# Optimization experiments

Measured on AMD Instinct MI355X. Metric: run time of the kernel, lower is better.

## Reference

```python
import jax, jax.numpy as jnp
import numpy as np

CL = 32      # config.cl (latent width)
NOBJ = 32    # config.num_obj
N = 1024     # batch


def _linear_params(key, fan_in, fan_out):
    w = jax.random.normal(key, (fan_in, fan_out), dtype=jnp.float32) / np.sqrt(fan_in)
    b = jnp.full((fan_out,), 0.1, dtype=jnp.float32)
    return w, b


def setup_inputs() -> dict:
    key = jax.random.key(0)
    keys = jax.random.split(key, 16)
    inp = {"s": jax.random.normal(keys[0], (N, NOBJ, CL // 2), dtype=jnp.float32)}
    specs = [
        ("state_enc", [(CL // 2, CL)]),
        ("self", [(CL, CL), (CL, CL)]),
        ("rel", [(2 * CL + 1, 2 * CL), (2 * CL, CL), (CL, CL)]),
        ("att", [(2 * CL + 1, 2 * CL), (2 * CL, CL), (CL, 1)]),
        ("aff", [(CL, CL), (CL, CL), (CL, CL)]),
        ("out", [(2 * CL, CL), (CL, CL)]),
    ]
    k = 1
    for name, shapes in specs:
        for j, (fi, fo) in enumerate(shapes):
            w, b = _linear_params(keys[k], fi, fo)
            k += 1
            if len(shapes) == 1:
                inp[name + "_w"], inp[name + "_b"] = w, b
            else:
                inp[name + "_w" + str(j)], inp[name + "_b" + str(j)] = w, b
    inp["core_idx"] = 0
    return inp


def _forward(s, state_enc_w, state_enc_b,
             self_w0, self_b0, self_w1, self_b1,
             rel_w0, rel_b0, rel_w1, rel_b1, rel_w2, rel_b2,
             att_w0, att_b0, att_w1, att_b1, att_w2, att_b2,
             aff_w0, aff_b0, aff_w1, aff_b1, aff_w2, aff_b2,
             out_w0, out_b0, out_w1, out_b1):
    # state encoding; keep raw (x, y) positions in the first 2 channels
    enc = s @ state_enc_w + state_enc_b                      # (n, o, cl)
    s2 = jnp.concatenate([s[..., :2], enc[..., 2:]], axis=-1)  # (n, o, cl)

    # self dynamics (residual MLP)
    h1 = jax.nn.relu(s2 @ self_w0 + self_b0)
    self_dyn = h1 @ self_w1 + self_b1 + h1                   # (n, o, cl)

    # pairwise squared distance over first two channels
    pos = s2[..., :2]
    diff = pos[:, :, None, :] - pos[:, None, :, :]           # (n, o, o, 2)
    dist = jnp.sum(diff * diff, axis=-1)                     # (n, o, o)

    # first layer of the edge MLPs applied to cat(obj_i, obj_j, dist) without
    # materializing the (n, o, o, 2cl+1) concat: split weight into W_i|W_j|w_d
    def pair_first(W, b):
        a = s2 @ W[:CL]                                      # (n, o, H)
        c = s2 @ W[CL:2 * CL]                                # (n, o, H)
        return a[:, :, None, :] + c[:, None, :, :] + dist[..., None] * W[2 * CL] + b

    # relation core (residual on last layer)
    rel1 = jax.nn.relu(pair_first(rel_w0, rel_b0))           # (n, o, o, 2cl)
    rel2 = jax.nn.relu(rel1 @ rel_w1 + rel_b1)               # (n, o, o, cl)
    rel_f = rel2 @ rel_w2 + rel_b2 + rel2                    # (n, o, o, cl)

    # attention net -> exp (unnormalized attention)
    att = jax.nn.relu(pair_first(att_w0, att_b0))
    att = jax.nn.relu(att @ att_w1 + att_b1)
    att = jnp.exp(att @ att_w2 + att_b2)                     # (n, o, o, 1)

    diag_mask = (1.0 - jnp.eye(NOBJ, dtype=s2.dtype))[None, :, :, None]
    rel_dyn = jnp.sum(rel_f * diag_mask * att, axis=2)       # (n, o, cl)

    dyn = self_dyn + rel_dyn

    # affector (tanh residual MLP)
    aff1 = jnp.tanh(dyn @ aff_w0 + aff_b0)
    aff2 = jnp.tanh(aff1 @ aff_w1 + aff_b1) + aff1
    aff3 = aff2 @ aff_w2 + aff_b2

    # output head
    aff_s = jnp.concatenate([aff3, s2], axis=-1)             # (n, o, 2cl)
    o1 = jnp.tanh(aff_s @ out_w0 + out_b0)
    result = o1 @ out_w1 + out_b1 + o1                       # (n, o, cl)
    return result


def reference(s, state_enc_w, state_enc_b,
              self_w0, self_b0, self_w1, self_b1,
              rel_w0, rel_b0, rel_w1, rel_b1, rel_w2, rel_b2,
              att_w0, att_b0, att_w1, att_b1, att_w2, att_b2,
              aff_w0, aff_b0, aff_w1, aff_b1, aff_w2, aff_b2,
              out_w0, out_b0, out_w1, out_b1, core_idx):
    # core_idx selects one of 3 identical cores in the original; only core 0
    # is materialized here (forward uses a single core).
    del core_idx
    return _forward(s, state_enc_w, state_enc_b,
                    self_w0, self_b0, self_w1, self_b1,
                    rel_w0, rel_b0, rel_w1, rel_b1, rel_w2, rel_b2,
                    att_w0, att_b0, att_w1, att_b1, att_w2, att_b2,
                    aff_w0, aff_b0, aff_w1, aff_b1, aff_w2, aff_b2,
                    out_w0, out_b0, out_w1, out_b1)
```

## Files before the change

### kernel.cpp

```cpp
#include <hip/hip_runtime.h>
#include <stdint.h>


enum : int {
  ENC_W  = 0,     ENC_B  = 512,
  SELF_W0 = 544,  SELF_B0 = 1568, SELF_W1 = 1600, SELF_B1 = 2624,
  REL_W0 = 2656,  REL_B0 = 6816,  REL_W1 = 6880,  REL_B1 = 8928,
  REL_W2 = 8960,  REL_B2 = 9984,
  ATT_W0 = 10016, ATT_B0 = 14176, ATT_W1 = 14240, ATT_B1 = 16288,
  ATT_W2 = 16320, ATT_B2 = 16352,
  AFF_W0 = 16356, AFF_B0 = 17380, AFF_W1 = 17412, AFF_B1 = 18436,
  AFF_W2 = 18468, AFF_B2 = 19492,
  OUT_W0 = 19524, OUT_B0 = 21572, OUT_W1 = 21604, OUT_B1 = 22628,
  W_FLAG = 22660,
  W_TOTAL = 22661
};

__device__ __forceinline__ float bf2f(uint16_t h) {
  union { uint32_t u; float f; } v; v.u = ((uint32_t)h) << 16; return v.f;
}
__device__ __forceinline__ uint16_t f2bf(float f) {
  union { float f; uint32_t u; } v; v.f = f;
  uint32_t r = (v.u + 0x7fffu + ((v.u >> 16) & 1u)) >> 16;
  return (uint16_t)r;
}

struct ConvArgs {
  const void* src[28];
  const uint32_t* probe;
  int size[28];
  int off[28];
};

__global__ void dyn_conv_kernel(ConvArgs a, float* __restrict__ W) {
  const int t = blockIdx.x;
  const bool is_fp32 = (*a.probe == 0x3DCCCCCDu);
  const int cnt = a.size[t];
  float* d = W + a.off[t];
  if (is_fp32) {
    const float* s = (const float*)a.src[t];
    for (int e = threadIdx.x; e < cnt; e += blockDim.x) d[e] = s[e];
  } else {
    const uint16_t* s = (const uint16_t*)a.src[t];
    for (int e = threadIdx.x; e < cnt; e += blockDim.x) d[e] = bf2f(s[e]);
  }
  if (t == 0 && threadIdx.x == 0) W[W_FLAG] = is_fp32 ? 1.f : 0.f;
}

struct ArenaPair {
  float pa[32][68];
  float pc[32][68];
};
struct ArenaPost {
  float rd[32][36];
  float t1[32][36];
  float t2[32][36];
};
struct ArenaEarly {
  float s[32][16];
  float h1[32][33];
};
union ArenaU {
  ArenaPair a;
  ArenaPost b;
  ArenaEarly c;
};

__global__ __launch_bounds__(256, 2) void dyn_main_kernel(
    const void* __restrict__ Sv,
    const float* __restrict__ Wf,
    void* __restrict__ OUTv)
{
  __shared__ __align__(16) ArenaU u;
  __shared__ float sh_s2[32][33];
  __shared__ float sh_dist[32][33];
  __shared__ float sh_sd[32][33];
  __shared__ float sh_wdr[64];
  __shared__ float sh_wda[64];
  __shared__ __align__(16) float shW1[2048];
  __shared__ float sh_misc[100];

  const int tid = threadIdx.x;
  const int n   = blockIdx.x;
  const int i8  = tid >> 3;
  const int l8  = tid & 7;
  const int m0  = l8 << 2;

  const bool is_fp32 = (Wf[W_FLAG] != 0.f);

  {
    const int e = tid * 2;
    if (is_fp32) {
      const float* sp = (const float*)Sv + (size_t)n * 512;
      u.c.s[e >> 4][e & 15]             = sp[e];
      u.c.s[(e + 1) >> 4][(e + 1) & 15] = sp[e + 1];
    } else {
      const uint16_t* sp = (const uint16_t*)Sv + (size_t)n * 512;
      u.c.s[e >> 4][e & 15]             = bf2f(sp[e]);
      u.c.s[(e + 1) >> 4][(e + 1) & 15] = bf2f(sp[e + 1]);
    }
  }
  __syncthreads();

  {
    float e0 = Wf[ENC_B + m0 + 0], e1 = Wf[ENC_B + m0 + 1];
    float e2 = Wf[ENC_B + m0 + 2], e3 = Wf[ENC_B + m0 + 3];
    #pragma unroll
    for (int c = 0; c < 16; ++c) {
      const float sc = u.c.s[i8][c];
      const float4 w = *(const float4*)&Wf[ENC_W + c * 32 + m0];
      e0 = fmaf(sc, w.x, e0); e1 = fmaf(sc, w.y, e1);
      e2 = fmaf(sc, w.z, e2); e3 = fmaf(sc, w.w, e3);
    }
    if (m0 == 0) { e0 = u.c.s[i8][0]; e1 = u.c.s[i8][1]; }
    sh_s2[i8][m0 + 0] = e0; sh_s2[i8][m0 + 1] = e1;
    sh_s2[i8][m0 + 2] = e2; sh_s2[i8][m0 + 3] = e3;
  }
  __syncthreads();

  {
    const float xi = sh_s2[i8][0], yi = sh_s2[i8][1];
    #pragma unroll
    for (int q = 0; q < 4; ++q) {
      const int j = m0 + q;
      const float dx = xi - sh_s2[j][0];
      const float dy = yi - sh_s2[j][1];
      sh_dist[i8][j] = dx * dx + dy * dy;
    }
  }
  {
    float a0 = Wf[SELF_B0 + m0 + 0], a1 = Wf[SELF_B0 + m0 + 1];
    float a2 = Wf[SELF_B0 + m0 + 2], a3 = Wf[SELF_B0 + m0 + 3];
    #pragma unroll
    for (int k = 0; k < 32; ++k) {
      const float x = sh_s2[i8][k];
      const float4 w = *(const float4*)&Wf[SELF_W0 + k * 32 + m0];
      a0 = fmaf(x, w.x, a0); a1 = fmaf(x, w.y, a1);
      a2 = fmaf(x, w.z, a2); a3 = fmaf(x, w.w, a3);
    }
    u.c.h1[i8][m0 + 0] = fmaxf(a0, 0.f); u.c.h1[i8][m0 + 1] = fmaxf(a1, 0.f);
    u.c.h1[i8][m0 + 2] = fmaxf(a2, 0.f); u.c.h1[i8][m0 + 3] = fmaxf(a3, 0.f);
  }
  __syncthreads();

  {
    float a0 = Wf[SELF_B1 + m0 + 0], a1 = Wf[SELF_B1 + m0 + 1];
    float a2 = Wf[SELF_B1 + m0 + 2], a3 = Wf[SELF_B1 + m0 + 3];
    #pragma unroll
    for (int k = 0; k < 32; ++k) {
      const float x = u.c.h1[i8][k];
      const float4 w = *(const float4*)&Wf[SELF_W1 + k * 32 + m0];
      a0 = fmaf(x, w.x, a0); a1 = fmaf(x, w.y, a1);
      a2 = fmaf(x, w.z, a2); a3 = fmaf(x, w.w, a3);
    }
    sh_sd[i8][m0 + 0] = a0 + u.c.h1[i8][m0 + 0];
    sh_sd[i8][m0 + 1] = a1 + u.c.h1[i8][m0 + 1];
    sh_sd[i8][m0 + 2] = a2 + u.c.h1[i8][m0 + 2];
    sh_sd[i8][m0 + 3] = a3 + u.c.h1[i8][m0 + 3];
  }
  __syncthreads();

  auto precompute_ac = [&](int W0base, int B0base) {
    const int arr = tid >> 7;
    const int row = (tid >> 2) & 31;
    const int k0  = (tid & 3) * 16;
    const float* bb = Wf + B0base + k0;
    const float bs = (arr == 0) ? 1.f : 0.f;
    float acc[16];
    #pragma unroll
    for (int kk = 0; kk < 16; ++kk) acc[kk] = bs * bb[kk];
    const float* wb = Wf + W0base + arr * 2048 + k0;
    for (int c = 0; c < 32; ++c) {
      const float sc = sh_s2[row][c];
      const float* w = wb + c * 64;
      #pragma unroll
      for (int kk = 0; kk < 16; kk += 4) {
        const float4 wv = *(const float4*)&w[kk];
        acc[kk + 0] = fmaf(sc, wv.x, acc[kk + 0]);
        acc[kk + 1] = fmaf(sc, wv.y, acc[kk + 1]);
        acc[kk + 2] = fmaf(sc, wv.z, acc[kk + 2]);
        acc[kk + 3] = fmaf(sc, wv.w, acc[kk + 3]);
      }
    }
    float* dst = (arr == 0) ? &u.a.pa[row][k0] : &u.a.pc[row][k0];
    #pragma unroll
    for (int kk = 0; kk < 16; kk += 4)
      *(float4*)&dst[kk] = make_float4(acc[kk], acc[kk+1], acc[kk+2], acc[kk+3]);
  };

  if (tid < 64)        sh_wdr[tid]      = Wf[REL_W0 + 64 * 64 + tid];
  else if (tid < 128)  sh_wda[tid - 64] = Wf[ATT_W0 + 64 * 64 + (tid - 64)];
  ((float4*)shW1)[tid]       = *(const float4*)&Wf[ATT_W1 + tid * 4];
  ((float4*)shW1)[tid + 256] = *(const float4*)&Wf[ATT_W1 + (tid + 256) * 4];
  if (tid < 97)
    sh_misc[tid] = Wf[tid < 32 ? REL_B1 + tid
                    : tid < 64 ? ATT_B1 + (tid - 32)
                    : tid < 96 ? ATT_W2 + (tid - 64) : ATT_B2];
  precompute_ac(ATT_W0, ATT_B0);
  __syncthreads();

  auto att_pair = [&](int p) -> float {
    asm volatile("" ::: "memory");
    const int j = l8 + 8 * p;
    const float d = sh_dist[i8][j];
    const float4* A = (const float4*)&u.a.pa[i8][0];
    const float4* C = (const float4*)&u.a.pc[j][0];
    const float4* D = (const float4*)&sh_wda[0];
    float v[32];
    #pragma unroll
    for (int m = 0; m < 32; ++m) v[m] = sh_misc[32 + m];
    #pragma unroll 1
    for (int kq = 0; kq < 16; ++kq) {
      const float4 av = A[kq], cv = C[kq], wv = D[kq];
      const float x0 = fmaxf(fmaf(d, wv.x, av.x + cv.x), 0.f);
      const float x1 = fmaxf(fmaf(d, wv.y, av.y + cv.y), 0.f);
      const float x2 = fmaxf(fmaf(d, wv.z, av.z + cv.z), 0.f);
      const float x3 = fmaxf(fmaf(d, wv.w, av.w + cv.w), 0.f);
      const float4* wb = (const float4*)shW1 + kq * 32;
      #pragma unroll
      for (int mq = 0; mq < 8; ++mq) {
        const float4 w0 = wb[mq], w1 = wb[8+mq], w2 = wb[16+mq], w3 = wb[24+mq];
        float t;
        t = fmaf(x0, w0.x, v[mq*4+0]); t = fmaf(x1, w1.x, t);
        t = fmaf(x2, w2.x, t);         v[mq*4+0] = fmaf(x3, w3.x, t);
        t = fmaf(x0, w0.y, v[mq*4+1]); t = fmaf(x1, w1.y, t);
        t = fmaf(x2, w2.y, t);         v[mq*4+1] = fmaf(x3, w3.y, t);
        t = fmaf(x0, w0.z, v[mq*4+2]); t = fmaf(x1, w1.z, t);
        t = fmaf(x2, w2.z, t);         v[mq*4+2] = fmaf(x3, w3.z, t);
        t = fmaf(x0, w0.w, v[mq*4+3]); t = fmaf(x1, w1.w, t);
        t = fmaf(x2, w2.w, t);         v[mq*4+3] = fmaf(x3, w3.w, t);
      }
    }
    float s0 = sh_misc[96], s1 = 0.f, s2 = 0.f, s3 = 0.f;
    #pragma unroll
    for (int k = 0; k < 32; k += 4) {
      s0 = fmaf(fmaxf(v[k + 0], 0.f), sh_misc[64 + k + 0], s0);
      s1 = fmaf(fmaxf(v[k + 1], 0.f), sh_misc[64 + k + 1], s1);
      s2 = fmaf(fmaxf(v[k + 2], 0.f), sh_misc[64 + k + 2], s2);
      s3 = fmaf(fmaxf(v[k + 3], 0.f), sh_misc[64 + k + 3], s3);
    }
    const float lg = (s0 + s1) + (s2 + s3);
    return (j == i8) ? 0.f : expf(lg);
  };
  const float e0 = att_pair(0);
  const float e1 = att_pair(1);
  const float e2 = att_pair(2);
  const float e3 = att_pair(3);
  float E = (e0 + e1) + (e2 + e3);
  __syncthreads();

  ((float4*)shW1)[tid]       = *(const float4*)&Wf[REL_W1 + tid * 4];
  ((float4*)shW1)[tid + 256] = *(const float4*)&Wf[REL_W1 + (tid + 256) * 4];
  precompute_ac(REL_W0, REL_B0);
  __syncthreads();

  float g[32];
  #pragma unroll
  for (int m = 0; m < 32; ++m) g[m] = 0.f;

  auto rel_pair = [&](int p, float e) {
    asm volatile("" ::: "memory");
    const int j = l8 + 8 * p;
    const float d = sh_dist[i8][j];
    const float4* A = (const float4*)&u.a.pa[i8][0];
    const float4* C = (const float4*)&u.a.pc[j][0];
    const float4* D = (const float4*)&sh_wdr[0];
    float v[32];
    #pragma unroll
    for (int m = 0; m < 32; ++m) v[m] = sh_misc[m];
    #pragma unroll 1
    for (int kq = 0; kq < 16; ++kq) {
      const float4 av = A[kq], cv = C[kq], wv = D[kq];
      const float x0 = fmaxf(fmaf(d, wv.x, av.x + cv.x), 0.f);
      const float x1 = fmaxf(fmaf(d, wv.y, av.y + cv.y), 0.f);
      const float x2 = fmaxf(fmaf(d, wv.z, av.z + cv.z), 0.f);
      const float x3 = fmaxf(fmaf(d, wv.w, av.w + cv.w), 0.f);
      const float4* wb = (const float4*)shW1 + kq * 32;
      #pragma unroll
      for (int mq = 0; mq < 8; ++mq) {
        const float4 w0 = wb[mq], w1 = wb[8+mq], w2 = wb[16+mq], w3 = wb[24+mq];
        float t;
        t = fmaf(x0, w0.x, v[mq*4+0]); t = fmaf(x1, w1.x, t);
        t = fmaf(x2, w2.x, t);         v[mq*4+0] = fmaf(x3, w3.x, t);
        t = fmaf(x0, w0.y, v[mq*4+1]); t = fmaf(x1, w1.y, t);
        t = fmaf(x2, w2.y, t);         v[mq*4+1] = fmaf(x3, w3.y, t);
        t = fmaf(x0, w0.z, v[mq*4+2]); t = fmaf(x1, w1.z, t);
        t = fmaf(x2, w2.z, t);         v[mq*4+2] = fmaf(x3, w3.z, t);
        t = fmaf(x0, w0.w, v[mq*4+3]); t = fmaf(x1, w1.w, t);
        t = fmaf(x2, w2.w, t);         v[mq*4+3] = fmaf(x3, w3.w, t);
      }
    }
    #pragma unroll
    for (int m = 0; m < 32; ++m)
      g[m] = fmaf(e, fmaxf(v[m], 0.f), g[m]);
  };
  rel_pair(0, e0);
  rel_pair(1, e1);
  rel_pair(2, e2);
  rel_pair(3, e3);

  #pragma unroll
  for (int m = 0; m < 32; ++m) {
    float vv = g[m];
    vv += __shfl_xor(vv, 1);
    vv += __shfl_xor(vv, 2);
    vv += __shfl_xor(vv, 4);
    g[m] = vv;
  }
  E += __shfl_xor(E, 1);
  E += __shfl_xor(E, 2);
  E += __shfl_xor(E, 4);
  __syncthreads();
  if (l8 == 0) {
    #pragma unroll
    for (int q = 0; q < 8; ++q)
      *(float4*)&u.b.t1[i8][q * 4] =
          make_float4(g[q * 4], g[q * 4 + 1], g[q * 4 + 2], g[q * 4 + 3]);
    u.b.t1[i8][32] = E;
  }
  __syncthreads();

  {
    const float Ei = u.b.t1[i8][32];
    float a0 = fmaf(Ei, Wf[REL_B2 + m0 + 0], u.b.t1[i8][m0 + 0]);
    float a1 = fmaf(Ei, Wf[REL_B2 + m0 + 1], u.b.t1[i8][m0 + 1]);
    float a2 = fmaf(Ei, Wf[REL_B2 + m0 + 2], u.b.t1[i8][m0 + 2]);
    float a3 = fmaf(Ei, Wf[REL_B2 + m0 + 3], u.b.t1[i8][m0 + 3]);
    #pragma unroll
    for (int k = 0; k < 32; ++k) {
      const float x = u.b.t1[i8][k];
      const float4 w = *(const float4*)&Wf[REL_W2 + k * 32 + m0];
      a0 = fmaf(x, w.x, a0); a1 = fmaf(x, w.y, a1);
      a2 = fmaf(x, w.z, a2); a3 = fmaf(x, w.w, a3);
    }
    __syncthreads();
    u.b.rd[i8][m0 + 0] = a0; u.b.rd[i8][m0 + 1] = a1;
    u.b.rd[i8][m0 + 2] = a2; u.b.rd[i8][m0 + 3] = a3;
  }
  __syncthreads();

  {
    float a0 = Wf[AFF_B0 + m0 + 0], a1 = Wf[AFF_B0 + m0 + 1];
    float a2 = Wf[AFF_B0 + m0 + 2], a3 = Wf[AFF_B0 + m0 + 3];
    #pragma unroll
    for (int k = 0; k < 32; ++k) {
      const float x = sh_sd[i8][k] + u.b.rd[i8][k];
      const float4 w = *(const float4*)&Wf[AFF_W0 + k * 32 + m0];
      a0 = fmaf(x, w.x, a0); a1 = fmaf(x, w.y, a1);
      a2 = fmaf(x, w.z, a2); a3 = fmaf(x, w.w, a3);
    }
    u.b.t1[i8][m0 + 0] = tanhf(a0); u.b.t1[i8][m0 + 1] = tanhf(a1);
    u.b.t1[i8][m0 + 2] = tanhf(a2); u.b.t1[i8][m0 + 3] = tanhf(a3);
  }
  __syncthreads();

  {
    float a0 = Wf[AFF_B1 + m0 + 0], a1 = Wf[AFF_B1 + m0 + 1];
    float a2 = Wf[AFF_B1 + m0 + 2], a3 = Wf[AFF_B1 + m0 + 3];
    #pragma unroll
    for (int k = 0; k < 32; ++k) {
      const float x = u.b.t1[i8][k];
      const float4 w = *(const float4*)&Wf[AFF_W1 + k * 32 + m0];
      a0 = fmaf(x, w.x, a0); a1 = fmaf(x, w.y, a1);
      a2 = fmaf(x, w.z, a2); a3 = fmaf(x, w.w, a3);
    }
    u.b.t2[i8][m0 + 0] = tanhf(a0) + u.b.t1[i8][m0 + 0];
    u.b.t2[i8][m0 + 1] = tanhf(a1) + u.b.t1[i8][m0 + 1];
    u.b.t2[i8][m0 + 2] = tanhf(a2) + u.b.t1[i8][m0 + 2];
    u.b.t2[i8][m0 + 3] = tanhf(a3) + u.b.t1[i8][m0 + 3];
  }
  __syncthreads();

  {
    float a0 = Wf[AFF_B2 + m0 + 0], a1 = Wf[AFF_B2 + m0 + 1];
    float a2 = Wf[AFF_B2 + m0 + 2], a3 = Wf[AFF_B2 + m0 + 3];
    #pragma unroll
    for (int k = 0; k < 32; ++k) {
      const float x = u.b.t2[i8][k];
      const float4 w = *(const float4*)&Wf[AFF_W2 + k * 32 + m0];
      a0 = fmaf(x, w.x, a0); a1 = fmaf(x, w.y, a1);
      a2 = fmaf(x, w.z, a2); a3 = fmaf(x, w.w, a3);
    }
    u.b.t1[i8][m0 + 0] = a0; u.b.t1[i8][m0 + 1] = a1;
    u.b.t1[i8][m0 + 2] = a2; u.b.t1[i8][m0 + 3] = a3;
  }
  __syncthreads();

  {
    float a0 = Wf[OUT_B0 + m0 + 0], a1 = Wf[OUT_B0 + m0 + 1];
    float a2 = Wf[OUT_B0 + m0 + 2], a3 = Wf[OUT_B0 + m0 + 3];
    #pragma unroll
    for (int k = 0; k < 32; ++k) {
      const float x1 = u.b.t1[i8][k];
      const float4 wa = *(const float4*)&Wf[OUT_W0 + k * 32 + m0];
      a0 = fmaf(x1, wa.x, a0); a1 = fmaf(x1, wa.y, a1);
      a2 = fmaf(x1, wa.z, a2); a3 = fmaf(x1, wa.w, a3);
      const float x2 = sh_s2[i8][k];
      const float4 wbv = *(const float4*)&Wf[OUT_W0 + (32 + k) * 32 + m0];
      a0 = fmaf(x2, wbv.x, a0); a1 = fmaf(x2, wbv.y, a1);
      a2 = fmaf(x2, wbv.z, a2); a3 = fmaf(x2, wbv.w, a3);
    }
    u.b.t2[i8][m0 + 0] = tanhf(a0); u.b.t2[i8][m0 + 1] = tanhf(a1);
    u.b.t2[i8][m0 + 2] = tanhf(a2); u.b.t2[i8][m0 + 3] = tanhf(a3);
  }
  __syncthreads();

  {
    float a0 = Wf[OUT_B1 + m0 + 0], a1 = Wf[OUT_B1 + m0 + 1];
    float a2 = Wf[OUT_B1 + m0 + 2], a3 = Wf[OUT_B1 + m0 + 3];
    #pragma unroll
    for (int k = 0; k < 32; ++k) {
      const float x = u.b.t2[i8][k];
      const float4 w = *(const float4*)&Wf[OUT_W1 + k * 32 + m0];
      a0 = fmaf(x, w.x, a0); a1 = fmaf(x, w.y, a1);
      a2 = fmaf(x, w.z, a2); a3 = fmaf(x, w.w, a3);
    }
    a0 += u.b.t2[i8][m0 + 0]; a1 += u.b.t2[i8][m0 + 1];
    a2 += u.b.t2[i8][m0 + 2]; a3 += u.b.t2[i8][m0 + 3];
    const size_t idx = (size_t)n * 1024 + i8 * 32 + m0;
    if (is_fp32) {
      *(float4*)&((float*)OUTv)[idx] = make_float4(a0, a1, a2, a3);
    } else {
      ushort4 r;
      r.x = f2bf(a0); r.y = f2bf(a1); r.z = f2bf(a2); r.w = f2bf(a3);
      *(ushort4*)&((uint16_t*)OUTv)[idx] = r;
    }
  }
}

extern "C" void kernel_launch(void* const* d_in, const int* in_sizes, int n_in,
                              void* d_out, int out_size, void* d_ws, size_t ws_size,
                              hipStream_t stream) {
  (void)in_sizes; (void)n_in; (void)out_size; (void)ws_size;
  static const int sizes[28] = {
    512, 32, 1024, 32, 1024, 32,
    4160, 64, 2048, 32, 1024, 32,
    4160, 64, 2048, 32, 32, 1,
    1024, 32, 1024, 32, 1024, 32,
    2048, 32, 1024, 32};
  static const int offs[28] = {
    ENC_W, ENC_B, SELF_W0, SELF_B0, SELF_W1, SELF_B1,
    REL_W0, REL_B0, REL_W1, REL_B1, REL_W2, REL_B2,
    ATT_W0, ATT_B0, ATT_W1, ATT_B1, ATT_W2, ATT_B2,
    AFF_W0, AFF_B0, AFF_W1, AFF_B1, AFF_W2, AFF_B2,
    OUT_W0, OUT_B0, OUT_W1, OUT_B1};

  ConvArgs ca;
  for (int i = 0; i < 28; ++i) {
    ca.src[i]  = d_in[1 + i];
    ca.size[i] = sizes[i];
    ca.off[i]  = offs[i];
  }
  ca.probe = (const uint32_t*)d_in[2];
  float* W = (float*)d_ws;
  hipLaunchKernelGGL(dyn_conv_kernel, dim3(28), dim3(256), 0, stream, ca, W);
  hipLaunchKernelGGL(dyn_main_kernel, dim3(1024), dim3(256), 0, stream,
                     d_in[0], (const float*)W, d_out);
}
```

Baseline: 376.5 us.

## Split pair MLP output channels across lane halves to halve accumulator registers

Reassigns the work of the attention and relation pair MLPs so that each lane computes 16 of the 32 hidden output channels for twice as many pairs (8 instead of 4), with lanes 0-3 and 4-7 splitting the channels. The attention logit is completed with one extra shuffle across the two halves, and the relation reduction and writeback are split between lanes 0 and 4. This lowers per-thread accumulator register use, which can raise occupancy or reduce spills. In exchange the x-activation computation (the relu of the first layer) is now done twice per pair, once in each half, and there are more serial pair iterations per lane.

```diff
diff --git a/kernel.cpp b/kernel.cpp
--- a/kernel.cpp
+++ b/kernel.cpp
@@ -85,6 +85,9 @@
   const int i8  = tid >> 3;
   const int l8  = tid & 7;
   const int m0  = l8 << 2;
+  const int jg  = l8 & 3;
+  const int h16 = (l8 >> 2) << 4;
+  const int h4  = (l8 >> 2) << 2;
 
   const bool is_fp32 = (Wf[W_FLAG] != 0.f);
 
@@ -201,14 +204,14 @@
 
   auto att_pair = [&](int p) -> float {
     asm volatile("" ::: "memory");
-    const int j = l8 + 8 * p;
+    const int j = jg + 4 * p;
     const float d = sh_dist[i8][j];
     const float4* A = (const float4*)&u.a.pa[i8][0];
     const float4* C = (const float4*)&u.a.pc[j][0];
     const float4* D = (const float4*)&sh_wda[0];
-    float v[32];
-    #pragma unroll
-    for (int m = 0; m < 32; ++m) v[m] = sh_misc[32 + m];
+    float v[16];
+    #pragma unroll
+    for (int m = 0; m < 16; ++m) v[m] = sh_misc[32 + h16 + m];
     #pragma unroll 1
     for (int kq = 0; kq < 16; ++kq) {
       const float4 av = A[kq], cv = C[kq], wv = D[kq];
@@ -216,9 +219,9 @@
       const float x1 = fmaxf(fmaf(d, wv.y, av.y + cv.y), 0.f);
       const float x2 = fmaxf(fmaf(d, wv.z, av.z + cv.z), 0.f);
       const float x3 = fmaxf(fmaf(d, wv.w, av.w + cv.w), 0.f);
-      const float4* wb = (const float4*)shW1 + kq * 32;
+      const float4* wb = (const float4*)shW1 + kq * 32 + h4;
       #pragma unroll
-      for (int mq = 0; mq < 8; ++mq) {
+      for (int mq = 0; mq < 4; ++mq) {
         const float4 w0 = wb[mq], w1 = wb[8+mq], w2 = wb[16+mq], w3 = wb[24+mq];
         float t;
         t = fmaf(x0, w0.x, v[mq*4+0]); t = fmaf(x1, w1.x, t);
@@ -231,22 +234,28 @@
         t = fmaf(x2, w2.w, t);         v[mq*4+3] = fmaf(x3, w3.w, t);
       }
     }
-    float s0 = sh_misc[96], s1 = 0.f, s2 = 0.f, s3 = 0.f;
-    #pragma unroll
-    for (int k = 0; k < 32; k += 4) {
-      s0 = fmaf(fmaxf(v[k + 0], 0.f), sh_misc[64 + k + 0], s0);
-      s1 = fmaf(fmaxf(v[k + 1], 0.f), sh_misc[64 + k + 1], s1);
-      s2 = fmaf(fmaxf(v[k + 2], 0.f), sh_misc[64 + k + 2], s2);
-      s3 = fmaf(fmaxf(v[k + 3], 0.f), sh_misc[64 + k + 3], s3);
-    }
-    const float lg = (s0 + s1) + (s2 + s3);
+    float s0 = 0.f, s1 = 0.f, s2 = 0.f, s3 = 0.f;
+    #pragma unroll
+    for (int k = 0; k < 16; k += 4) {
+      s0 = fmaf(fmaxf(v[k + 0], 0.f), sh_misc[64 + h16 + k + 0], s0);
+      s1 = fmaf(fmaxf(v[k + 1], 0.f), sh_misc[64 + h16 + k + 1], s1);
+      s2 = fmaf(fmaxf(v[k + 2], 0.f), sh_misc[64 + h16 + k + 2], s2);
+      s3 = fmaf(fmaxf(v[k + 3], 0.f), sh_misc[64 + h16 + k + 3], s3);
+    }
+    float lg = (s0 + s1) + (s2 + s3);
+    lg += __shfl_xor(lg, 4);
+    lg += sh_misc[96];
     return (j == i8) ? 0.f : expf(lg);
   };
   const float e0 = att_pair(0);
   const float e1 = att_pair(1);
   const float e2 = att_pair(2);
   const float e3 = att_pair(3);
-  float E = (e0 + e1) + (e2 + e3);
+  const float e4 = att_pair(4);
+  const float e5 = att_pair(5);
+  const float e6 = att_pair(6);
+  const float e7 = att_pair(7);
+  float E = ((e0 + e1) + (e2 + e3)) + ((e4 + e5) + (e6 + e7));
   __syncthreads();
 
   ((float4*)shW1)[tid]       = *(const float4*)&Wf[REL_W1 + tid * 4];
@@ -254,20 +263,20 @@
   precompute_ac(REL_W0, REL_B0);
   __syncthreads();
 
-  float g[32];
+  float g[16];
   #pragma unroll
-  for (int m = 0; m < 32; ++m) g[m] = 0.f;
+  for (int m = 0; m < 16; ++m) g[m] = 0.f;
 
   auto rel_pair = [&](int p, float e) {
     asm volatile("" ::: "memory");
-    const int j = l8 + 8 * p;
+    const int j = jg + 4 * p;
     const float d = sh_dist[i8][j];
     const float4* A = (const float4*)&u.a.pa[i8][0];
     const float4* C = (const float4*)&u.a.pc[j][0];
     const float4* D = (const float4*)&sh_wdr[0];
-    float v[32];
-    #pragma unroll
-    for (int m = 0; m < 32; ++m) v[m] = sh_misc[m];
+    float v[16];
+    #pragma unroll
+    for (int m = 0; m < 16; ++m) v[m] = sh_misc[h16 + m];
     #pragma unroll 1
     for (int kq = 0; kq < 16; ++kq) {
       const float4 av = A[kq], cv = C[kq], wv = D[kq];
@@ -275,9 +284,9 @@
       const float x1 = fmaxf(fmaf(d, wv.y, av.y + cv.y), 0.f);
       const float x2 = fmaxf(fmaf(d, wv.z, av.z + cv.z), 0.f);
       const float x3 = fmaxf(fmaf(d, wv.w, av.w + cv.w), 0.f);
-      const float4* wb = (const float4*)shW1 + kq * 32;
+      const float4* wb = (const float4*)shW1 + kq * 32 + h4;
       #pragma unroll
-      for (int mq = 0; mq < 8; ++mq) {
+      for (int mq = 0; mq < 4; ++mq) {
         const float4 w0 = wb[mq], w1 = wb[8+mq], w2 = wb[16+mq], w3 = wb[24+mq];
         float t;
         t = fmaf(x0, w0.x, v[mq*4+0]); t = fmaf(x1, w1.x, t);
@@ -291,32 +300,39 @@
       }
     }
     #pragma unroll
-    for (int m = 0; m < 32; ++m)
+    for (int m = 0; m < 16; ++m)
       g[m] = fmaf(e, fmaxf(v[m], 0.f), g[m]);
   };
   rel_pair(0, e0);
   rel_pair(1, e1);
   rel_pair(2, e2);
   rel_pair(3, e3);
+  rel_pair(4, e4);
+  rel_pair(5, e5);
+  rel_pair(6, e6);
+  rel_pair(7, e7);
 
   #pragma unroll
-  for (int m = 0; m < 32; ++m) {
+  for (int m = 0; m < 16; ++m) {
     float vv = g[m];
     vv += __shfl_xor(vv, 1);
     vv += __shfl_xor(vv, 2);
-    vv += __shfl_xor(vv, 4);
     g[m] = vv;
   }
   E += __shfl_xor(E, 1);
   E += __shfl_xor(E, 2);
-  E += __shfl_xor(E, 4);
   __syncthreads();
   if (l8 == 0) {
     #pragma unroll
-    for (int q = 0; q < 8; ++q)
+    for (int q = 0; q < 4; ++q)
       *(float4*)&u.b.t1[i8][q * 4] =
           make_float4(g[q * 4], g[q * 4 + 1], g[q * 4 + 2], g[q * 4 + 3]);
     u.b.t1[i8][32] = E;
+  } else if (l8 == 4) {
+    #pragma unroll
+    for (int q = 0; q < 4; ++q)
+      *(float4*)&u.b.t1[i8][16 + q * 4] =
+          make_float4(g[q * 4], g[q * 4 + 1], g[q * 4 + 2], g[q * 4 + 3]);
   }
   __syncthreads();
 
```

New measurement: 388.5 us. 3.2% more time.

## Stage dense-layer weights into double-buffered shared memory ahead of use

Applied to the files above, without the earlier changes.

Adds a second 2048-float shared weight buffer. Each layer's weights are copied from global memory into one buffer while the current layer reads from the other, so the matvec loops read float4 weights from LDS instead of global/L1. The copies are placed in the phase before each layer, so load latency is hidden behind the preceding barrier-separated stage. This costs 8 KB more LDS per block, which may lower occupancy below the two blocks the launch bounds ask for.

```diff
diff --git a/kernel.cpp b/kernel.cpp
--- a/kernel.cpp
+++ b/kernel.cpp
@@ -77,7 +77,8 @@
   __shared__ float sh_sd[32][33];
   __shared__ float sh_wdr[64];
   __shared__ float sh_wda[64];
-  __shared__ __align__(16) float shW1[2048];
+  __shared__ __align__(16) float sh_wtA[2048];
+  __shared__ __align__(16) float sh_wtB[2048];
   __shared__ float sh_misc[100];
 
   const int tid = threadIdx.x;
@@ -87,6 +88,15 @@
   const int m0  = l8 << 2;
 
   const bool is_fp32 = (Wf[W_FLAG] != 0.f);
+
+  const float4* wtA4 = (const float4*)sh_wtA;
+  const float4* wtB4 = (const float4*)sh_wtB;
+
+  auto stage = [&](float* dst, int off, int n4) {
+    const float4* src = (const float4*)(Wf + off);
+    float4* d4 = (float4*)dst;
+    for (int q = tid; q < n4; q += 256) d4[q] = src[q];
+  };
 
   {
     const int e = tid * 2;
@@ -99,6 +109,7 @@
       u.c.s[e >> 4][e & 15]             = bf2f(sp[e]);
       u.c.s[(e + 1) >> 4][(e + 1) & 15] = bf2f(sp[e + 1]);
     }
+    stage(sh_wtA, ENC_W, 128);
   }
   __syncthreads();
 
@@ -108,13 +119,14 @@
     #pragma unroll
     for (int c = 0; c < 16; ++c) {
       const float sc = u.c.s[i8][c];
-      const float4 w = *(const float4*)&Wf[ENC_W + c * 32 + m0];
+      const float4 w = wtA4[c * 8 + l8];
       e0 = fmaf(sc, w.x, e0); e1 = fmaf(sc, w.y, e1);
       e2 = fmaf(sc, w.z, e2); e3 = fmaf(sc, w.w, e3);
     }
     if (m0 == 0) { e0 = u.c.s[i8][0]; e1 = u.c.s[i8][1]; }
     sh_s2[i8][m0 + 0] = e0; sh_s2[i8][m0 + 1] = e1;
     sh_s2[i8][m0 + 2] = e2; sh_s2[i8][m0 + 3] = e3;
+    stage(sh_wtB, SELF_W0, 256);
   }
   __syncthreads();
 
@@ -134,12 +146,13 @@
     #pragma unroll
     for (int k = 0; k < 32; ++k) {
       const float x = sh_s2[i8][k];
-      const float4 w = *(const float4*)&Wf[SELF_W0 + k * 32 + m0];
+      const float4 w = wtB4[k * 8 + l8];
       a0 = fmaf(x, w.x, a0); a1 = fmaf(x, w.y, a1);
       a2 = fmaf(x, w.z, a2); a3 = fmaf(x, w.w, a3);
     }
     u.c.h1[i8][m0 + 0] = fmaxf(a0, 0.f); u.c.h1[i8][m0 + 1] = fmaxf(a1, 0.f);
     u.c.h1[i8][m0 + 2] = fmaxf(a2, 0.f); u.c.h1[i8][m0 + 3] = fmaxf(a3, 0.f);
+    stage(sh_wtA, SELF_W1, 256);
   }
   __syncthreads();
 
@@ -149,7 +162,7 @@
     #pragma unroll
     for (int k = 0; k < 32; ++k) {
       const float x = u.c.h1[i8][k];
-      const float4 w = *(const float4*)&Wf[SELF_W1 + k * 32 + m0];
+      const float4 w = wtA4[k * 8 + l8];
       a0 = fmaf(x, w.x, a0); a1 = fmaf(x, w.y, a1);
       a2 = fmaf(x, w.z, a2); a3 = fmaf(x, w.w, a3);
     }
@@ -190,8 +203,7 @@
 
   if (tid < 64)        sh_wdr[tid]      = Wf[REL_W0 + 64 * 64 + tid];
   else if (tid < 128)  sh_wda[tid - 64] = Wf[ATT_W0 + 64 * 64 + (tid - 64)];
-  ((float4*)shW1)[tid]       = *(const float4*)&Wf[ATT_W1 + tid * 4];
-  ((float4*)shW1)[tid + 256] = *(const float4*)&Wf[ATT_W1 + (tid + 256) * 4];
+  stage(sh_wtB, ATT_W1, 512);
   if (tid < 97)
     sh_misc[tid] = Wf[tid < 32 ? REL_B1 + tid
                     : tid < 64 ? ATT_B1 + (tid - 32)
@@ -199,6 +211,7 @@
   precompute_ac(ATT_W0, ATT_B0);
   __syncthreads();
 
+  stage(sh_wtA, REL_W1, 512);
   auto att_pair = [&](int p) -> float {
     asm volatile("" ::: "memory");
     const int j = l8 + 8 * p;
@@ -216,7 +229,7 @@
       const float x1 = fmaxf(fmaf(d, wv.y, av.y + cv.y), 0.f);
       const float x2 = fmaxf(fmaf(d, wv.z, av.z + cv.z), 0.f);
       const float x3 = fmaxf(fmaf(d, wv.w, av.w + cv.w), 0.f);
-      const float4* wb = (const float4*)shW1 + kq * 32;
+      const float4* wb = wtB4 + kq * 32;
       #pragma unroll
       for (int mq = 0; mq < 8; ++mq) {
         const float4 w0 = wb[mq], w1 = wb[8+mq], w2 = wb[16+mq], w3 = wb[24+mq];
@@ -249,9 +262,8 @@
   float E = (e0 + e1) + (e2 + e3);
   __syncthreads();
 
-  ((float4*)shW1)[tid]       = *(const float4*)&Wf[REL_W1 + tid * 4];
-  ((float4*)shW1)[tid + 256] = *(const float4*)&Wf[REL_W1 + (tid + 256) * 4];
   precompute_ac(REL_W0, REL_B0);
+  stage(sh_wtB, REL_W2, 256);
   __syncthreads();
 
   float g[32];
@@ -275,7 +287,7 @@
       const float x1 = fmaxf(fmaf(d, wv.y, av.y + cv.y), 0.f);
       const float x2 = fmaxf(fmaf(d, wv.z, av.z + cv.z), 0.f);
       const float x3 = fmaxf(fmaf(d, wv.w, av.w + cv.w), 0.f);
-      const float4* wb = (const float4*)shW1 + kq * 32;
+      const float4* wb = wtA4 + kq * 32;
       #pragma unroll
       for (int mq = 0; mq < 8; ++mq) {
         const float4 w0 = wb[mq], w1 = wb[8+mq], w2 = wb[16+mq], w3 = wb[24+mq];
@@ -321,6 +333,7 @@
   __syncthreads();
 
   {
+    stage(sh_wtA, AFF_W0, 256);
     const float Ei = u.b.t1[i8][32];
     float a0 = fmaf(Ei, Wf[REL_B2 + m0 + 0], u.b.t1[i8][m0 + 0]);
     float a1 = fmaf(Ei, Wf[REL_B2 + m0 + 1], u.b.t1[i8][m0 + 1]);
@@ -329,7 +342,7 @@
     #pragma unroll
     for (int k = 0; k < 32; ++k) {
       const float x = u.b.t1[i8][k];
-      const float4 w = *(const float4*)&Wf[REL_W2 + k * 32 + m0];
+      const float4 w = wtB4[k * 8 + l8];
       a0 = fmaf(x, w.x, a0); a1 = fmaf(x, w.y, a1);
       a2 = fmaf(x, w.z, a2); a3 = fmaf(x, w.w, a3);
     }
@@ -340,12 +353,13 @@
   __syncthreads();
 
   {
+    stage(sh_wtB, AFF_W1, 256);
     float a0 = Wf[AFF_B0 + m0 + 0], a1 = Wf[AFF_B0 + m0 + 1];
     float a2 = Wf[AFF_B0 + m0 + 2], a3 = Wf[AFF_B0 + m0 + 3];
     #pragma unroll
     for (int k = 0; k < 32; ++k) {
       const float x = sh_sd[i8][k] + u.b.rd[i8][k];
-      const float4 w = *(const float4*)&Wf[AFF_W0 + k * 32 + m0];
+      const float4 w = wtA4[k * 8 + l8];
       a0 = fmaf(x, w.x, a0); a1 = fmaf(x, w.y, a1);
       a2 = fmaf(x, w.z, a2); a3 = fmaf(x, w.w, a3);
     }
@@ -355,12 +369,13 @@
   __syncthreads();
 
   {
+    stage(sh_wtA, AFF_W2, 256);
     float a0 = Wf[AFF_B1 + m0 + 0], a1 = Wf[AFF_B1 + m0 + 1];
     float a2 = Wf[AFF_B1 + m0 + 2], a3 = Wf[AFF_B1 + m0 + 3];
     #pragma unroll
     for (int k = 0; k < 32; ++k) {
       const float x = u.b.t1[i8][k];
-      const float4 w = *(const float4*)&Wf[AFF_W1 + k * 32 + m0];
+      const float4 w = wtB4[k * 8 + l8];
       a0 = fmaf(x, w.x, a0); a1 = fmaf(x, w.y, a1);
       a2 = fmaf(x, w.z, a2); a3 = fmaf(x, w.w, a3);
     }
@@ -372,12 +387,13 @@
   __syncthreads();
 
   {
+    stage(sh_wtB, OUT_W0, 512);
     float a0 = Wf[AFF_B2 + m0 + 0], a1 = Wf[AFF_B2 + m0 + 1];
     float a2 = Wf[AFF_B2 + m0 + 2], a3 = Wf[AFF_B2 + m0 + 3];
     #pragma unroll
     for (int k = 0; k < 32; ++k) {
       const float x = u.b.t2[i8][k];
-      const float4 w = *(const float4*)&Wf[AFF_W2 + k * 32 + m0];
+      const float4 w = wtA4[k * 8 + l8];
       a0 = fmaf(x, w.x, a0); a1 = fmaf(x, w.y, a1);
       a2 = fmaf(x, w.z, a2); a3 = fmaf(x, w.w, a3);
     }
@@ -387,16 +403,17 @@
   __syncthreads();
 
   {
+    stage(sh_wtA, OUT_W1, 256);
     float a0 = Wf[OUT_B0 + m0 + 0], a1 = Wf[OUT_B0 + m0 + 1];
     float a2 = Wf[OUT_B0 + m0 + 2], a3 = Wf[OUT_B0 + m0 + 3];
     #pragma unroll
     for (int k = 0; k < 32; ++k) {
       const float x1 = u.b.t1[i8][k];
-      const float4 wa = *(const float4*)&Wf[OUT_W0 + k * 32 + m0];
+      const float4 wa = wtB4[k * 8 + l8];
       a0 = fmaf(x1, wa.x, a0); a1 = fmaf(x1, wa.y, a1);
       a2 = fmaf(x1, wa.z, a2); a3 = fmaf(x1, wa.w, a3);
       const float x2 = sh_s2[i8][k];
-      const float4 wbv = *(const float4*)&Wf[OUT_W0 + (32 + k) * 32 + m0];
+      const float4 wbv = wtB4[256 + k * 8 + l8];
       a0 = fmaf(x2, wbv.x, a0); a1 = fmaf(x2, wbv.y, a1);
       a2 = fmaf(x2, wbv.z, a2); a3 = fmaf(x2, wbv.w, a3);
     }
@@ -411,7 +428,7 @@
     #pragma unroll
     for (int k = 0; k < 32; ++k) {
       const float x = u.b.t2[i8][k];
-      const float4 w = *(const float4*)&Wf[OUT_W1 + k * 32 + m0];
+      const float4 w = wtA4[k * 8 + l8];
       a0 = fmaf(x, w.x, a0); a1 = fmaf(x, w.y, a1);
       a2 = fmaf(x, w.z, a2); a3 = fmaf(x, w.w, a3);
     }
```

After: 363.5 us. 3.4% less time.
